# Performance work log

Hardware: AMD Instinct MI355X
Metric: run time of the kernel (lower is better)

## Reference

```python
import jax, jax.numpy as jnp
import numpy as np

NUM_TOPICS = 50
NUM_TIMES = 12
VOCAB1 = 5000
VOCAB2 = 2000
T_HIDDEN = 400
RHO = 300
DELTA = 0.005
BATCH = 32


def setup_inputs() -> dict:
    key = jax.random.key(0)
    ks = jax.random.split(key, 16)
    s = 0.02
    V = VOCAB1 + VOCAB2
    d = {}
    d["bows"] = jax.random.uniform(ks[0], (BATCH, NUM_TIMES, V), jnp.float32)
    d["normalized_bows"] = jax.random.uniform(ks[1], (BATCH, NUM_TIMES, V), jnp.float32)
    d["qmap_w"] = jax.random.normal(ks[2], (T_HIDDEN, V), jnp.float32) * s
    d["qmap_b"] = jnp.zeros((T_HIDDEN,), jnp.float32)
    d["lstm_wih0"] = jax.random.normal(ks[3], (4 * T_HIDDEN, T_HIDDEN), jnp.float32) * s
    d["lstm_whh0"] = jax.random.normal(ks[4], (4 * T_HIDDEN, T_HIDDEN), jnp.float32) * s
    d["lstm_bih0"] = jnp.zeros((4 * T_HIDDEN,), jnp.float32)
    d["lstm_bhh0"] = jnp.zeros((4 * T_HIDDEN,), jnp.float32)
    d["lstm_wih1"] = jax.random.normal(ks[5], (4 * T_HIDDEN, T_HIDDEN), jnp.float32) * s
    d["lstm_whh1"] = jax.random.normal(ks[6], (4 * T_HIDDEN, T_HIDDEN), jnp.float32) * s
    d["lstm_bih1"] = jnp.zeros((4 * T_HIDDEN,), jnp.float32)
    d["lstm_bhh1"] = jnp.zeros((4 * T_HIDDEN,), jnp.float32)
    d["mu_theta_w"] = jax.random.normal(ks[7], (NUM_TOPICS, T_HIDDEN + NUM_TOPICS), jnp.float32) * s
    d["mu_theta_b"] = jnp.zeros((NUM_TOPICS,), jnp.float32)
    d["ls_theta_w"] = jax.random.normal(ks[8], (NUM_TOPICS, T_HIDDEN + NUM_TOPICS), jnp.float32) * s
    d["ls_theta_b"] = jnp.zeros((NUM_TOPICS,), jnp.float32)
    d["mu_q_alpha"] = jax.random.normal(ks[9], (NUM_TOPICS, NUM_TIMES, RHO), jnp.float32)
    d["logsigma_q_alpha"] = jax.random.normal(ks[10], (NUM_TOPICS, NUM_TIMES, RHO), jnp.float32)
    d["rho1_w"] = jax.random.normal(ks[11], (VOCAB1, RHO), jnp.float32) * s
    d["rho1_b"] = jnp.zeros((VOCAB1,), jnp.float32)
    d["rho2_w"] = jax.random.normal(ks[12], (VOCAB2, RHO), jnp.float32) * s
    d["rho2_b"] = jnp.zeros((VOCAB2,), jnp.float32)
    return d


def _kl(qm, qls, pm, pls):
    # 0.5 * sum_last[ (exp(qls) + (qm-pm)^2) / (exp(pls)+1e-6) - 1 + pls - qls ], mean over rest
    t = (jnp.exp(qls) + (qm - pm) ** 2) / (jnp.exp(pls) + 1e-6) - 1.0 + pls - qls
    return (0.5 * jnp.sum(t, axis=-1)).mean()


def _lstm(x, layers):
    # x: [B, T, H]; PyTorch gate order i, f, g, o; eval mode -> no inter-layer dropout
    for wih, whh, bih, bhh in layers:
        B = x.shape[0]
        H = whh.shape[1]

        def step(carry, xt, wih=wih, whh=whh, bih=bih, bhh=bhh):
            h, c = carry
            g = xt @ wih.T + bih + h @ whh.T + bhh
            i, f, gg, o = jnp.split(g, 4, axis=-1)
            c = jax.nn.sigmoid(f) * c + jax.nn.sigmoid(i) * jnp.tanh(gg)
            h = jax.nn.sigmoid(o) * jnp.tanh(c)
            return (h, c), h

        init = (jnp.zeros((B, H), x.dtype), jnp.zeros((B, H), x.dtype))
        _, hs = jax.lax.scan(step, init, jnp.swapaxes(x, 0, 1))  # [T, B, H]
        x = jnp.swapaxes(hs, 0, 1)
    return x


def _likelihood(beta, theta, bows_v, key):
    # beta: [T, K, V], theta: [T, B, K], bows_v: [B, T, V]
    def body(carry, xs):
        t, beta_t, theta_t, bows_t = xs
        # pi[b,v,k] = softmax_k( beta[k,v] * theta[b,k] )
        pi = jax.nn.softmax(theta_t[:, None, :] * beta_t.T[None, :, :], axis=-1)  # [B,V,K]
        g = jax.random.gumbel(jax.random.fold_in(key, t), pi.shape, pi.dtype)
        # F.gumbel_softmax with pi as the "logits", tau=1, hard=True (straight-through)
        y_soft = jax.nn.softmax(pi + g, axis=-1)
        y_hard = jax.nn.one_hot(jnp.argmax(y_soft, axis=-1), pi.shape[-1], dtype=pi.dtype)
        z = y_hard + y_soft - jax.lax.stop_gradient(y_soft)
        kld = (-(z * jnp.log(theta_t)[:, None, :]).sum(-1).mean()
               - (((pi * z).sum(-1) * (jnp.log(pi) * z).sum(-1)).sum(-1)).mean())
        beta_z = beta_t * z.mean(0).T   # [K, V]
        theta_z = theta_t * z.mean(1)   # [B, K]
        ll = (jnp.log(theta_z @ beta_z) * bows_t).sum(1).mean()
        return carry, (kld, ll)

    ts = jnp.arange(beta.shape[0])
    _, (klds, lls) = jax.lax.scan(jax.checkpoint(body), 0,
                                  (ts, beta, theta, jnp.swapaxes(bows_v, 0, 1)))
    return klds.sum(), lls.sum()


def _forward(bows, normalized_bows, qmap_w, qmap_b,
             lstm_wih0, lstm_whh0, lstm_bih0, lstm_bhh0,
             lstm_wih1, lstm_whh1, lstm_bih1, lstm_bhh1,
             mu_theta_w, mu_theta_b, ls_theta_w, ls_theta_b,
             mu_q_alpha, logsigma_q_alpha, rho1_w, rho1_b, rho2_w, rho2_b):
    B = bows.shape[0]
    log_delta = jnp.log(jnp.float32(DELTA))

    # ---- get_theta (eval mode: reparameterize -> mu, dropout off) ----
    inp = normalized_bows @ qmap_w.T + qmap_b                       # [B,T,H]
    out = _lstm(inp, [(lstm_wih0, lstm_whh0, lstm_bih0, lstm_bhh0),
                      (lstm_wih1, lstm_whh1, lstm_bih1, lstm_bhh1)])
    out_t = jnp.swapaxes(out, 0, 1)                                 # [T,B,H]
    inp0 = jnp.concatenate([out_t[0], jnp.zeros((B, NUM_TOPICS), out.dtype)], axis=-1)
    mu0 = inp0 @ mu_theta_w.T + mu_theta_b
    ls0 = inp0 @ ls_theta_w.T + ls_theta_b
    kl0 = _kl(mu0, ls0, jnp.zeros_like(mu0), jnp.zeros_like(ls0))

    def tstep(z_prev, o_t):
        inp_t = jnp.concatenate([o_t, z_prev], axis=-1)
        mu = inp_t @ mu_theta_w.T + mu_theta_b
        ls = inp_t @ ls_theta_w.T + ls_theta_b
        klt = _kl(mu, ls, z_prev, jnp.full_like(mu, log_delta))
        return mu, (mu, klt)

    _, (zs_rest, kls) = jax.lax.scan(tstep, mu0, out_t[1:])
    zs = jnp.concatenate([mu0[None], zs_rest], axis=0)              # [T,B,K]
    kld_theta = kl0 + kls.sum()
    theta = jax.nn.softmax(zs, axis=-1)

    # ---- get_alpha (eval mode: alpha_t = mu_q_alpha[:,t]) -> fully vectorized ----
    q_mu = jnp.swapaxes(mu_q_alpha, 0, 1)                           # [T,K,R]
    q_ls = jnp.swapaxes(logsigma_q_alpha, 0, 1)
    p_mu = jnp.concatenate([jnp.zeros_like(q_mu[:1]), q_mu[:-1]], axis=0)
    p_ls = jnp.concatenate([jnp.zeros_like(q_ls[:1]), jnp.full_like(q_ls[1:], log_delta)], axis=0)
    kl_tk = 0.5 * jnp.sum((jnp.exp(q_ls) + (q_mu - p_mu) ** 2) / (jnp.exp(p_ls) + 1e-6)
                          - 1.0 + p_ls - q_ls, axis=-1)             # [T,K]
    kld_alpha = kl_tk.mean(-1).sum()
    alpha = q_mu

    # ---- get_beta ----
    beta1 = jax.nn.softmax(jnp.einsum('tkr,vr->tkv', alpha, rho1_w) + rho1_b, axis=-1)
    beta2 = jax.nn.softmax(jnp.einsum('tkr,vr->tkv', alpha, rho2_w) + rho2_b, axis=-1)

    # ---- decode ----
    key = jax.random.key(42)
    kld_z1, ll1 = _likelihood(beta1, theta, bows[:, :, :VOCAB1], jax.random.fold_in(key, 1))
    kld_z2, ll2 = _likelihood(beta2, theta, bows[:, :, -VOCAB2:], jax.random.fold_in(key, 2))
    recon_loss = -ll1 - ll2
    return jnp.stack([recon_loss, kld_theta, kld_z1, kld_z2, kld_alpha])


def reference(bows, normalized_bows, qmap_w, qmap_b,
              lstm_wih0, lstm_whh0, lstm_bih0, lstm_bhh0,
              lstm_wih1, lstm_whh1, lstm_bih1, lstm_bhh1,
              mu_theta_w, mu_theta_b, ls_theta_w, ls_theta_b,
              mu_q_alpha, logsigma_q_alpha, rho1_w, rho1_b, rho2_w, rho2_b):
    return _forward(bows, normalized_bows, qmap_w, qmap_b,
                    lstm_wih0, lstm_whh0, lstm_bih0, lstm_bhh0,
                    lstm_wih1, lstm_whh1, lstm_bih1, lstm_bhh1,
                    mu_theta_w, mu_theta_b, ls_theta_w, ls_theta_b,
                    mu_q_alpha, logsigma_q_alpha, rho1_w, rho1_b, rho2_w, rho2_b)
```

## Files before the change

kernel.cpp:

```cpp
#include <hip/hip_runtime.h>

#define LOG_DELTA (-5.2983174f)
#define LOG50     (3.9120230054f)

typedef __attribute__((ext_vector_type(8))) short short8v;
typedef __attribute__((ext_vector_type(4))) float f32x4;

constexpr size_t OFF_C1G1  = 0;
constexpr size_t OFF_C1G2  = 19200;
constexpr size_t OFF_ACCS  = 38400;
constexpr size_t OFF_C0G   = 38416;
constexpr size_t OFF_BETA  = OFF_C0G  + 4200000;
constexpr size_t OFF_ALPHAT= OFF_BETA + 4200000;
constexpr size_t OFF_INP   = OFF_ALPHAT + 180000;
constexpr size_t OFF_X0    = OFF_INP  + 153600;
constexpr size_t OFF_OUT0  = OFF_X0   + 614400;
constexpr size_t OFF_X1    = OFF_OUT0 + 153600;
constexpr size_t OFF_OUT1  = OFF_X1   + 614400;
constexpr size_t OFF_CST   = OFF_OUT1 + 153600;
constexpr size_t OFF_MUH   = OFF_CST  + 12800;
constexpr size_t OFF_THETA = OFF_MUH  + 38400;
constexpr size_t OFF_LTH   = OFF_THETA+ 19200;
constexpr size_t OFF_MUW4  = OFF_LTH  + 19200;
constexpr size_t OFF_LSW4  = OFF_MUW4 + 20000;
constexpr size_t OFF_RS    = OFF_LTH  + 3300;
constexpr size_t OFF_W0T   = OFF_C0G;
constexpr size_t OFF_W1T   = OFF_C0G + 640000;
constexpr size_t OFF_WIH1T = OFF_C0G + 1280000;
constexpr size_t OFF_NBBF  = OFF_C0G + 1920000;
constexpr size_t OFF_R1BF  = OFF_C0G + 3271680;
constexpr size_t OFF_QWBF  = OFF_BETA;
constexpr size_t OFF_W0BF  = OFF_BETA + 1408000;
constexpr size_t OFF_CST1  = OFF_X1;
constexpr size_t OFF_ALBF  = OFF_X1 + 12800;
constexpr size_t OFF_R2BF  = OFF_X1 + 108800;

__device__ __forceinline__ float wsum64(float x){
  #pragma unroll
  for (int o = 32; o; o >>= 1) x += __shfl_down(x, o);
  return x;
}
__device__ __forceinline__ float u01(unsigned int x){
  x ^= x >> 16; x *= 0x7feb352dU;
  x ^= x >> 15; x *= 0x846ca68bU;
  x ^= x >> 16;
  return ((float)x + 0.5f) * (1.0f/4294967296.0f);
}
__device__ __forceinline__ unsigned short f2bf(float x){
  unsigned int u = __float_as_uint(x);
  u += 0x7FFFu + ((u >> 16) & 1u);
  return (unsigned short)(u >> 16);
}
__device__ __forceinline__ ushort4 f4bf(float4 v){
  ushort4 r;
  r.x = f2bf(v.x); r.y = f2bf(v.y); r.z = f2bf(v.z); r.w = f2bf(v.w);
  return r;
}

__global__ void prep_misc(float* __restrict__ ws,
    const float* __restrict__ muW, const float* __restrict__ lsW,
    const float* __restrict__ qmu,
    const float* __restrict__ bi0, const float* __restrict__ bh0,
    const float* __restrict__ bi1, const float* __restrict__ bh1,
    const float* __restrict__ mb,  const float* __restrict__ lb,
    const float* __restrict__ qb,
    const float* __restrict__ whh0, const float* __restrict__ whh1,
    const float* __restrict__ wih1,
    const float* __restrict__ nbows, const float* __restrict__ qmap_w,
    const float* __restrict__ wih0,
    const float* __restrict__ rho1w, const float* __restrict__ rho2w)
{
  float* zbase = ws + OFF_C1G1;
  float* muW4  = ws + OFF_MUW4;
  float* lsW4  = ws + OFF_LSW4;
  unsigned short* albf = (unsigned short*)(ws + OFF_ALBF);
  float* bsum0 = ws + OFF_LTH;
  float* bsum1 = ws + OFF_LTH + 1600;
  float* mlb   = ws + OFF_LTH + 3200;
  float* rs    = ws + OFF_RS;
  unsigned int* inbz = (unsigned int*)(ws + OFF_INP);
  float* inpf  = ws + OFF_ALPHAT;
  float* w0T   = ws + OFF_W0T;
  float* w1T   = ws + OFF_W1T;
  float* wi1T  = ws + OFF_WIH1T;
  unsigned short* nbbf = (unsigned short*)(ws + OFF_NBBF);
  unsigned short* qwbf = (unsigned short*)(ws + OFF_QWBF);
  unsigned short* w0bf = (unsigned short*)(ws + OFF_W0BF);
  unsigned short* r1bf = (unsigned short*)(ws + OFF_R1BF);
  unsigned short* r2bf = (unsigned short*)(ws + OFF_R2BF);
  const float4 z4 = {0.f, 0.f, 0.f, 0.f};

  for (long long un = blockIdx.x*blockDim.x + threadIdx.x; un < 2713337LL;
       un += (long long)gridDim.x*blockDim.x){
    if (un < 9604){
      int j = (int)un * 4;
      if (j + 3 < 38416) *(float4*)&zbase[j] = z4;
      else { for (int q = 0; q < 4 && j+q < 38416; ++q) zbase[j+q] = 0.f; }
    }
    else if (un < 14604){
      int j = (int)(un - 9604) * 4;
      int k = j / 400, c = j % 400;
      const float* s = &muW[k*450 + c];
      float4 v = {s[0], s[1], s[2], s[3]};
      *(float4*)&muW4[j] = v;
    }
    else if (un < 19604){
      int j = (int)(un - 14604) * 4;
      int k = j / 400, c = j % 400;
      const float* s = &lsW[k*450 + c];
      float4 v = {s[0], s[1], s[2], s[3]};
      *(float4*)&lsW4[j] = v;
    }
    else if (un < 67604){
      int j = (int)(un - 19604) * 4;
      int m = j / 320, r = j % 320;
      int t = m / 50, k = m % 50;
      ushort4 o = {0,0,0,0};
      if (r < 300) o = f4bf(*(const float4*)&qmu[((size_t)k*12 + t)*300 + r]);
      *(ushort4*)&albf[j] = o;
    }
    else if (un < 68004){
      int j = (int)(un - 67604) * 4;
      float4 a = *(const float4*)&bi0[j], b = *(const float4*)&bh0[j];
      float4 v = {a.x+b.x, a.y+b.y, a.z+b.z, a.w+b.w};
      *(float4*)&bsum0[j] = v;
    }
    else if (un < 68404){
      int j = (int)(un - 68004) * 4;
      float4 a = *(const float4*)&bi1[j], b = *(const float4*)&bh1[j];
      float4 v = {a.x+b.x, a.y+b.y, a.z+b.z, a.w+b.w};
      *(float4*)&bsum1[j] = v;
    }
    else if (un < 68429){
      int j = (int)(un - 68404) * 4;
      #pragma unroll
      for (int q = 0; q < 4; ++q){
        int jj = j + q;
        mlb[jj] = (jj < 50) ? mb[jj] : lb[jj-50];
      }
    }
    else if (un < 68729){
      int j = (int)(un - 68429) * 4;
      *(float4*)&rs[j] = z4;
    }
    else if (un < 88697){
      int j = (int)(un - 68729) * 4;
      *(uint4*)&inbz[j] = make_uint4(0u,0u,0u,0u);
    }
    else if (un < 568697){
      long long rel = un - 88697;
      int half = (int)(rel / 160000);
      int j = (int)(rel % 160000) * 4;
      int r = j / 1600, c = j % 1600;
      int u = c >> 2;
      const float* src = (half == 0) ? whh0 : (half == 1) ? whh1 : wih1;
      float* dst = (half == 0) ? w0T : (half == 1) ? w1T : wi1T;
      float4 v = { src[((size_t)(0*400 + u))*400 + r],
                   src[((size_t)(1*400 + u))*400 + r],
                   src[((size_t)(2*400 + u))*400 + r],
                   src[((size_t)(3*400 + u))*400 + r] };
      *(float4*)&dst[j] = v;
    }
    else if (un < 1244537){
      int j = (int)(un - 568697) * 4;
      int row = j / 7040, v = j % 7040;
      ushort4 o = {0,0,0,0};
      if (v < 7000) o = f4bf(*(const float4*)&nbows[(size_t)row*7000 + v]);
      *(ushort4*)&nbbf[j] = o;
    }
    else if (un < 1948537){
      int j = (int)(un - 1244537) * 4;
      int row = j / 7040, v = j % 7040;
      ushort4 o = {0,0,0,0};
      if (v < 7000) o = f4bf(*(const float4*)&qmap_w[(size_t)row*7000 + v]);
      *(ushort4*)&qwbf[j] = o;
    }
    else if (un < 2114937){
      int j = (int)(un - 1948537) * 4;
      int row = j / 416, r = j % 416;
      ushort4 o = {0,0,0,0};
      if (r < 400) o = f4bf(*(const float4*)&wih0[(size_t)row*400 + r]);
      *(ushort4*)&w0bf[j] = o;
    }
    else if (un < 2514937){
      int j = (int)(un - 2114937) * 4;
      int row = j / 320, r = j % 320;
      ushort4 o = {0,0,0,0};
      if (r < 300) o = f4bf(*(const float4*)&rho1w[(size_t)row*300 + r]);
      *(ushort4*)&r1bf[j] = o;
    }
    else if (un < 2674937){
      int j = (int)(un - 2514937) * 4;
      int row = j / 320, r = j % 320;
      ushort4 o = {0,0,0,0};
      if (r < 300) o = f4bf(*(const float4*)&rho2w[(size_t)row*300 + r]);
      *(ushort4*)&r2bf[j] = o;
    }
    else {
      int j = (int)(un - 2674937) * 4;
      int c = j % 400;
      *(float4*)&inpf[j] = *(const float4*)&qb[c];
    }
  }
}

__global__ __launch_bounds__(256) void gemm_bf16(
    const unsigned short* __restrict__ A, int lda,
    const unsigned short* __restrict__ B, int ldb,
    float* __restrict__ Cf, unsigned short* __restrict__ Cbf,
    float* __restrict__ Cacc, int ldc,
    int M, int N, int Kp, int kchunk,
    const float* __restrict__ bias, float* __restrict__ rowsum)
{
  __shared__ unsigned short As[64][40];
  __shared__ unsigned short Bs[64][40];
  __shared__ float sexp[64];
  const int tid = threadIdx.x;
  const int m0 = blockIdx.y * 64, n0 = blockIdx.x * 64;
  const int kbeg = blockIdx.z * kchunk;
  const int kend = min(Kp, kbeg + kchunk);
  const int wave = tid >> 6, lane = tid & 63;
  const int wm = (wave >> 1) * 32, wn = (wave & 1) * 32;
  const int ra = tid >> 2, ck = (tid & 3) << 3;
  const int fr = lane & 15, fo = (lane >> 4) << 3;
  if (rowsum && tid < 64) sexp[tid] = 0.f;

  f32x4 acc00 = {0.f,0.f,0.f,0.f}, acc01 = {0.f,0.f,0.f,0.f};
  f32x4 acc10 = {0.f,0.f,0.f,0.f}, acc11 = {0.f,0.f,0.f,0.f};
  int4 pa, pb;
  {
    int rA = m0 + ra, rB = n0 + ra;
    pa = (rA < M) ? *(const int4*)&A[(size_t)rA*lda + kbeg + ck] : make_int4(0,0,0,0);
    pb = (rB < N) ? *(const int4*)&B[(size_t)rB*ldb + kbeg + ck] : make_int4(0,0,0,0);
  }
  for (int k0 = kbeg; k0 < kend; k0 += 32){
    *(int4*)&As[ra][ck] = pa;
    *(int4*)&Bs[ra][ck] = pb;
    __syncthreads();
    if (k0 + 32 < kend){
      int rA = m0 + ra, rB = n0 + ra;
      pa = (rA < M) ? *(const int4*)&A[(size_t)rA*lda + k0 + 32 + ck] : make_int4(0,0,0,0);
      pb = (rB < N) ? *(const int4*)&B[(size_t)rB*ldb + k0 + 32 + ck] : make_int4(0,0,0,0);
    }
    short8v a0 = *(const short8v*)&As[wm      + fr][fo];
    short8v a1 = *(const short8v*)&As[wm + 16 + fr][fo];
    short8v b0 = *(const short8v*)&Bs[wn      + fr][fo];
    short8v b1 = *(const short8v*)&Bs[wn + 16 + fr][fo];
    acc00 = __builtin_amdgcn_mfma_f32_16x16x32_bf16(a0, b0, acc00, 0, 0, 0);
    acc01 = __builtin_amdgcn_mfma_f32_16x16x32_bf16(a0, b1, acc01, 0, 0, 0);
    acc10 = __builtin_amdgcn_mfma_f32_16x16x32_bf16(a1, b0, acc10, 0, 0, 0);
    acc11 = __builtin_amdgcn_mfma_f32_16x16x32_bf16(a1, b1, acc11, 0, 0, 0);
    __syncthreads();
  }
  const int rbase = (lane >> 4) << 2;
  auto epi = [&](f32x4 ac0, f32x4 ac1, int mi){
    #pragma unroll
    for (int reg = 0; reg < 4; ++reg){
      const int lr = wm + mi*16 + rbase + reg;
      const int gr = m0 + lr;
      float ex = 0.f;
      {
        int gc = n0 + wn + fr;
        if (gr < M && gc < N){
          if (Cacc) atomicAdd(&Cacc[(size_t)gr*ldc + gc], ac0[reg]);
          else {
            float val = ac0[reg] + (bias ? bias[gc] : 0.f);
            if (Cbf) Cbf[(size_t)gr*ldc + gc] = f2bf(val);
            else     Cf [(size_t)gr*ldc + gc] = val;
            if (rowsum) ex += __expf(val);
          }
        }
      }
      {
        int gc = n0 + wn + 16 + fr;
        if (gr < M && gc < N){
          if (Cacc) atomicAdd(&Cacc[(size_t)gr*ldc + gc], ac1[reg]);
          else {
            float val = ac1[reg] + (bias ? bias[gc] : 0.f);
            if (Cbf) Cbf[(size_t)gr*ldc + gc] = f2bf(val);
            else     Cf [(size_t)gr*ldc + gc] = val;
            if (rowsum) ex += __expf(val);
          }
        }
      }
      if (rowsum){
        ex += __shfl_xor(ex, 1); ex += __shfl_xor(ex, 2);
        ex += __shfl_xor(ex, 4); ex += __shfl_xor(ex, 8);
        if (fr == 0 && gr < M) atomicAdd(&sexp[lr], ex);
      }
    }
  };
  epi(acc00, acc01, 0);
  epi(acc10, acc11, 1);
  if (rowsum){
    __syncthreads();
    if (tid < 64 && m0 + tid < M) atomicAdd(&rowsum[m0 + tid], sexp[tid]);
  }
}

__global__ void cvt_inp(const float* __restrict__ inpf, unsigned short* __restrict__ inpbf){
  int un = blockIdx.x*blockDim.x + threadIdx.x;
  if (un < 38400){
    int j = un * 4;
    int r = j / 400, c = j % 400;
    ushort4 o = f4bf(*(const float4*)&inpf[j]);
    *(ushort4*)&inpbf[r*416 + c] = o;
  }
}

__device__ __forceinline__ float4 g4(const float* __restrict__ base, int row, int nrows,
                                     int ld, int k, int kend){
  float4 v; v.x = v.y = v.z = v.w = 0.f;
  if (row < nrows){
    const float* q = base + (size_t)row*ld + k;
    if (k + 3 < kend) v = *(const float4*)q;
  }
  return v;
}
__global__ __launch_bounds__(256) void gemm_f32(
    const float* __restrict__ A, int lda,
    const float* __restrict__ B, int ldb,
    float* __restrict__ C, int ldc,
    int M, int N, int K,
    const float* __restrict__ bias)
{
  __shared__ __align__(16) float As[16][68];
  __shared__ __align__(16) float Bs[16][68];
  const int tid = threadIdx.x;
  const int m0 = blockIdx.y * 64, n0 = blockIdx.x * 64;
  const int lm  = tid >> 2;
  const int lkq = (tid & 3) << 2;
  const int ty = tid >> 4, tx = tid & 15;
  float acc[4][4];
  #pragma unroll
  for (int i=0;i<4;++i)
    #pragma unroll
    for (int j=0;j<4;++j) acc[i][j] = 0.f;
  for (int k0 = 0; k0 < K; k0 += 16){
    float4 av = g4(A, m0+lm, M, lda, k0+lkq, K);
    float4 bv = g4(B, n0+lm, N, ldb, k0+lkq, K);
    As[lkq+0][lm]=av.x; As[lkq+1][lm]=av.y; As[lkq+2][lm]=av.z; As[lkq+3][lm]=av.w;
    Bs[lkq+0][lm]=bv.x; Bs[lkq+1][lm]=bv.y; Bs[lkq+2][lm]=bv.z; Bs[lkq+3][lm]=bv.w;
    __syncthreads();
    #pragma unroll
    for (int kk = 0; kk < 16; ++kk){
      const float4 a = *(const float4*)&As[kk][ty<<2];
      const float4 b = *(const float4*)&Bs[kk][tx<<2];
      float ar[4] = {a.x,a.y,a.z,a.w};
      float br[4] = {b.x,b.y,b.z,b.w};
      #pragma unroll
      for (int i=0;i<4;++i)
        #pragma unroll
        for (int j=0;j<4;++j) acc[i][j] = fmaf(ar[i], br[j], acc[i][j]);
    }
    __syncthreads();
  }
  const int om = m0 + (ty<<2), on = n0 + (tx<<2);
  #pragma unroll
  for (int i=0;i<4;++i)
    #pragma unroll
    for (int j=0;j<4;++j)
      if (om+i < M && on+j < N)
        C[(size_t)(om+i)*ldc + (on+j)] = acc[i][j] + (bias ? bias[on+j] : 0.f);
}

__global__ __launch_bounds__(256) void lstm_pipe(
    const float* __restrict__ X0,    const float* __restrict__ w0T,
    const float* __restrict__ wi1T,  const float* __restrict__ w1T,
    const float* __restrict__ bsum1,
    float* __restrict__ hs0, float* __restrict__ hs1,
    float* __restrict__ cst0, float* __restrict__ cst1, int step)
{
  __shared__ __align__(16) float4 hq4[100*32];
  __shared__ __align__(16) float4 red4[4][32][2];
  const int tid = threadIdx.x;
  const int rh = tid >> 6;
  const int b  = (tid & 63) >> 1;
  const int ul = tid & 1;
  const int rq0 = rh * 25;

  if (blockIdx.x < 200){
    const int t = step;
    if (t >= 12) return;
    const int U0 = blockIdx.x * 2;
    const int u = U0 + ul;
    if (t > 0){
      for (int i = tid; i < 3200; i += 256){
        int bb = i & 31, rq = i >> 5;
        hq4[rq*32 + bb] = *(const float4*)&hs0[((size_t)(bb*12 + (t-1)))*400 + rq*4];
      }
      __syncthreads();
      const float* wcol = w0T + (size_t)u*4;
      float4 acc = {0.f,0.f,0.f,0.f};
      #pragma unroll 5
      for (int rq = rq0; rq < rq0 + 25; ++rq){
        float4 h4 = hq4[rq*32 + b];
        float hr[4] = {h4.x, h4.y, h4.z, h4.w};
        #pragma unroll
        for (int dr = 0; dr < 4; ++dr){
          float4 w4 = *(const float4*)&wcol[(size_t)(rq*4 + dr)*1600];
          acc.x = fmaf(hr[dr], w4.x, acc.x);
          acc.y = fmaf(hr[dr], w4.y, acc.y);
          acc.z = fmaf(hr[dr], w4.z, acc.z);
          acc.w = fmaf(hr[dr], w4.w, acc.w);
        }
      }
      red4[rh][b][ul] = acc;
    }
    __syncthreads();
    if (tid < 64){
      const int bb = tid >> 1, uu = U0 + (tid & 1);
      float4 a = {0.f,0.f,0.f,0.f};
      if (t > 0){
        #pragma unroll
        for (int w = 0; w < 4; ++w){
          float4 r = red4[w][bb][tid & 1];
          a.x += r.x; a.y += r.y; a.z += r.z; a.w += r.w;
        }
      }
      const size_t xrow = ((size_t)bb*12 + t)*1600;
      float gi = a.x + X0[xrow          + uu];
      float gf = a.y + X0[xrow +  400   + uu];
      float gg = a.z + X0[xrow +  800   + uu];
      float go = a.w + X0[xrow + 1200   + uu];
      float ii = 1.f/(1.f + expf(-gi));
      float ff = 1.f/(1.f + expf(-gf));
      float tg = tanhf(gg);
      float oo = 1.f/(1.f + expf(-go));
      float c = (t == 0) ? 0.f : cst0[bb*400 + uu];
      c = ff*c + ii*tg;
      cst0[bb*400 + uu] = c;
      hs0[((size_t)bb*12 + t)*400 + uu] = oo * tanhf(c);
    }
  } else {
    const int t = step - 1;
    if (t < 0) return;
    const int U0 = (blockIdx.x - 200) * 2;
    const int u = U0 + ul;
    float4 acc = {0.f,0.f,0.f,0.f};
    for (int i = tid; i < 3200; i += 256){
      int bb = i & 31, rq = i >> 5;
      hq4[rq*32 + bb] = *(const float4*)&hs0[((size_t)(bb*12 + t))*400 + rq*4];
    }
    __syncthreads();
    {
      const float* wcol = wi1T + (size_t)u*4;
      #pragma unroll 5
      for (int rq = rq0; rq < rq0 + 25; ++rq){
        float4 h4 = hq4[rq*32 + b];
        float hr[4] = {h4.x, h4.y, h4.z, h4.w};
        #pragma unroll
        for (int dr = 0; dr < 4; ++dr){
          float4 w4 = *(const float4*)&wcol[(size_t)(rq*4 + dr)*1600];
          acc.x = fmaf(hr[dr], w4.x, acc.x);
          acc.y = fmaf(hr[dr], w4.y, acc.y);
          acc.z = fmaf(hr[dr], w4.z, acc.z);
          acc.w = fmaf(hr[dr], w4.w, acc.w);
        }
      }
    }
    __syncthreads();
    if (t > 0){
      for (int i = tid; i < 3200; i += 256){
        int bb = i & 31, rq = i >> 5;
        hq4[rq*32 + bb] = *(const float4*)&hs1[((size_t)(bb*12 + (t-1)))*400 + rq*4];
      }
    }
    __syncthreads();
    if (t > 0){
      const float* wcol = w1T + (size_t)u*4;
      #pragma unroll 5
      for (int rq = rq0; rq < rq0 + 25; ++rq){
        float4 h4 = hq4[rq*32 + b];
        float hr[4] = {h4.x, h4.y, h4.z, h4.w};
        #pragma unroll
        for (int dr = 0; dr < 4; ++dr){
          float4 w4 = *(const float4*)&wcol[(size_t)(rq*4 + dr)*1600];
          acc.x = fmaf(hr[dr], w4.x, acc.x);
          acc.y = fmaf(hr[dr], w4.y, acc.y);
          acc.z = fmaf(hr[dr], w4.z, acc.z);
          acc.w = fmaf(hr[dr], w4.w, acc.w);
        }
      }
    }
    red4[rh][b][ul] = acc;
    __syncthreads();
    if (tid < 64){
      const int bb = tid >> 1, uu = U0 + (tid & 1);
      float4 a = {0.f,0.f,0.f,0.f};
      #pragma unroll
      for (int w = 0; w < 4; ++w){
        float4 r = red4[w][bb][tid & 1];
        a.x += r.x; a.y += r.y; a.z += r.z; a.w += r.w;
      }
      float gi = a.x + bsum1[        uu];
      float gf = a.y + bsum1[ 400 + uu];
      float gg = a.z + bsum1[ 800 + uu];
      float go = a.w + bsum1[1200 + uu];
      float ii = 1.f/(1.f + expf(-gi));
      float ff = 1.f/(1.f + expf(-gf));
      float tg = tanhf(gg);
      float oo = 1.f/(1.f + expf(-go));
      float c = (t == 0) ? 0.f : cst1[bb*400 + uu];
      c = ff*c + ii*tg;
      cst1[bb*400 + uu] = c;
      hs1[((size_t)bb*12 + t)*400 + uu] = oo * tanhf(c);
    }
  }
}

__global__ __launch_bounds__(512) void theta_par(
    const float* __restrict__ muH2,
    const float* __restrict__ muW, const float* __restrict__ lsW,
    float* __restrict__ theta, float* __restrict__ accs)
{
  __shared__ float zsall[12][8][50];
  __shared__ float wm[50][51], wl[50][51];
  __shared__ float ktot;
  const int tid = threadIdx.x;
  const int b0 = blockIdx.x * 8;
  for (int i = tid; i < 2500; i += 512){
    int k = i / 50, j = i % 50;
    wm[k][j] = muW[k*450 + 400 + j];
    wl[k][j] = lsW[k*450 + 400 + j];
  }
  if (tid == 0) ktot = 0.f;
  __syncthreads();
  const float dd = expf(LOG_DELTA) + 1e-6f;
  for (int t = 0; t < 12; ++t){
    float kpart = 0.f;
    if (tid < 400){
      int bl = tid / 50, k = tid % 50, b = b0 + bl;
      float m = muH2[((size_t)b*12 + t)*100 + k];
      float l = muH2[((size_t)b*12 + t)*100 + 50 + k];
      float zp = 0.f;
      if (t > 0){
        zp = zsall[t-1][bl][k];
        float sm = 0.f, sl = 0.f;
        #pragma unroll 5
        for (int j = 0; j < 50; ++j){
          float z = zsall[t-1][bl][j];
          sm = fmaf(z, wm[k][j], sm);
          sl = fmaf(z, wl[k][j], sl);
        }
        m += sm; l += sl;
      }
      zsall[t][bl][k] = m;
      float denom = (t > 0) ? dd : (1.f + 1e-6f);
      float pls = (t > 0) ? LOG_DELTA : 0.f;
      float d = m - zp;
      kpart += (expf(l) + d*d)/denom - 1.f + pls - l;
    }
    kpart = wsum64(kpart);
    if ((tid & 63) == 0) atomicAdd(&ktot, 0.5f * kpart / 32.f);
    __syncthreads();
  }
  for (int rr = tid; rr < 96; rr += 512){
    int t = rr >> 3, bl = rr & 7, b = b0 + bl;
    float m = -3.0e38f;
    for (int k = 0; k < 50; ++k) m = fmaxf(m, zsall[t][bl][k]);
    float S = 0.f;
    for (int k = 0; k < 50; ++k) S += expf(zsall[t][bl][k] - m);
    float inv = 1.f/S;
    for (int k = 0; k < 50; ++k)
      theta[((size_t)t*32 + b)*50 + k] = expf(zsall[t][bl][k] - m) * inv;
  }
  if (tid == 0) atomicAdd(&accs[6], ktot);
}

__global__ void kld_alpha_k(const float* __restrict__ qmu, const float* __restrict__ qls,
                            float* __restrict__ accs){
  const int t = blockIdx.x / 50, k = blockIdx.x % 50;
  const size_t base  = ((size_t)k*12 + t)*300;
  const size_t pbase = ((size_t)k*12 + (t-1))*300;
  const float dd  = (t > 0) ? (expf(LOG_DELTA) + 1e-6f) : (1.f + 1e-6f);
  const float pls = (t > 0) ? LOG_DELTA : 0.f;
  float s = 0.f;
  for (int r = threadIdx.x; r < 300; r += 64){
    float qm = qmu[base + r], ql = qls[base + r];
    float pm = (t > 0) ? qmu[pbase + r] : 0.f;
    float d = qm - pm;
    s += (expf(ql) + d*d)/dd - 1.f + pls - ql;
  }
  s = wsum64(s);
  if (threadIdx.x == 0) atomicAdd(&accs[7], 0.5f * s / 50.f);
}

__global__ __launch_bounds__(256) void pass1(
    const float* __restrict__ blog, const float* __restrict__ rs,
    const float* __restrict__ theta,
    float* __restrict__ bzg,
    float* __restrict__ c1g1, float* __restrict__ c1g2,
    float* __restrict__ accs)
{
  const int t = blockIdx.y;
  const int v0 = blockIdx.x * 64;
  __shared__ float th[32][50];
  __shared__ float be[50][64];
  __shared__ float c0s[64][50];
  __shared__ unsigned int c1p[2][32][25];
  __shared__ float rlog[2][50];
  __shared__ float kred[4];
  const int tid = threadIdx.x;

  if (tid < 100){
    int p = tid / 50, k = tid % 50;
    rlog[p][k] = __logf(rs[p*600 + t*50 + k]);
  }
  float lg[13];
  #pragma unroll
  for (int j = 0; j < 13; ++j){
    int i = tid + j*256;
    lg[j] = -40.f;
    if (i < 3200){
      int k = i >> 6, vl = i & 63, v = v0 + vl;
      if (v < 7000) lg[j] = blog[((size_t)t*50 + k)*7000 + v];
    }
  }
  #pragma unroll
  for (int j = 0; j < 7; ++j){
    int i = tid + j*256;
    if (i < 1600) th[i/50][i%50] = theta[(size_t)t*1600 + i];
  }
  #pragma unroll
  for (int j = 0; j < 13; ++j){
    int i = tid + j*256;
    if (i < 3200) ((float*)c0s)[i] = 0.f;
  }
  #pragma unroll
  for (int j = 0; j < 7; ++j){
    int i = tid + j*256;
    if (i < 1600) ((unsigned int*)c1p)[i] = 0u;
  }
  if (tid < 4) kred[tid] = 0.f;
  __syncthreads();
  #pragma unroll
  for (int j = 0; j < 13; ++j){
    int i = tid + j*256;
    if (i < 3200){
      int k = i >> 6, vl = i & 63, v = v0 + vl;
      int p = (v >= 5000);
      be[k][vl] = __expf(lg[j] - rlog[p][k]);
    }
  }
  __syncthreads();

  const int b = tid >> 3, sub = tid & 7;

  float sx[8], mx[8];
  #pragma unroll
  for (int i = 0; i < 8; ++i){ sx[i] = 0.f; mx[i] = 0.f; }
  for (int k = 0; k < 50; ++k){
    float tk = th[b][k];
    #pragma unroll
    for (int i = 0; i < 8; ++i){
      float x = tk * be[k][sub + 8*i];
      sx[i] += x;
      mx[i] = fmaxf(mx[i], x);
    }
  }
  float inv[8], lS1[8], bnd[8];
  #pragma unroll
  for (int i = 0; i < 8; ++i){
    inv[i] = 1.f / (50.f + sx[i]);
    lS1[i] = LOG50 + sx[i] * 0.02f;
    bnd[i] = (1.f + mx[i]) * inv[i];
  }

  int ks[8]; float xs[8];
  unsigned fmask = 0;
  const int vbase = (t*32 + b)*7000 + v0 + sub;
  #pragma unroll
  for (int i = 0; i < 8; ++i){
    ks[i] = 0; xs[i] = 0.f;
    if (v0 + sub + 8*i >= 7000) fmask |= 1u << i;
  }
  int round = 0;
  while (true){
    const unsigned roff = (unsigned)round * 0x9E3779B9u;
    #pragma unroll
    for (int i = 0; i < 8; ++i){
      if (!((fmask >> i) & 1u)){
        const unsigned bse = (unsigned)(vbase + 8*i) * 2u;
        float u1 = u01(bse + roff);
        float u2 = u01(bse + 1u + roff);
        int kp = min((int)(u1 * 50.f), 49);
        float x  = th[b][kp] * be[kp][sub + 8*i];
        float pi = (1.f + x) * inv[i];
        float y  = pi - bnd[i];
        float ap = 1.f + y + 0.5f*y*y;
        if (u2 <= ap || round >= 7){
          ks[i] = kp; xs[i] = x; fmask |= 1u << i;
        }
      }
    }
    ++round;
    if (__all(fmask == 255u)) break;
  }

  float kA1 = 0.f, kB1 = 0.f, kA2 = 0.f, kB2 = 0.f;
  #pragma unroll
  for (int i = 0; i < 8; ++i){
    const int vl = sub + 8*i, v = v0 + vl;
    if (v < 7000){
      float pis  = (1.f + xs[i]) * inv[i];
      float lpis = xs[i] - lS1[i];
      float lt   = __logf(th[b][ks[i]]);
      if (v >= 5000){ kA2 += lt; kB2 += pis*lpis; }
      else          { kA1 += lt; kB1 += pis*lpis; }
      atomicAdd(&c0s[vl][ks[i]], 1.f);
      atomicAdd(&c1p[(v >= 5000) ? 1 : 0][b][ks[i] >> 1],
                (ks[i] & 1) ? 65536u : 1u);
    }
  }
  kA1 = wsum64(kA1); kB1 = wsum64(kB1); kA2 = wsum64(kA2); kB2 = wsum64(kB2);
  if ((tid & 63) == 0){
    atomicAdd(&kred[0], kA1); atomicAdd(&kred[1], kB1);
    atomicAdd(&kred[2], kA2); atomicAdd(&kred[3], kB2);
  }
  __syncthreads();
  #pragma unroll
  for (int j = 0; j < 13; ++j){
    int i = tid + j*256;
    if (i < 3200){
      int k = i >> 6, vl = i & 63, v = v0 + vl;
      if (v < 7000)
        bzg[(size_t)t*350000 + (size_t)k*7000 + v] = be[k][vl] * c0s[vl][k] * (1.f/32.f);
    }
  }
  for (int i = tid; i < 1600; i += 256){
    int b2 = i / 50, k2 = i % 50;
    unsigned w1 = c1p[0][b2][k2 >> 1];
    unsigned w2 = c1p[1][b2][k2 >> 1];
    unsigned cnt1 = (k2 & 1) ? (w1 >> 16) : (w1 & 0xFFFFu);
    unsigned cnt2 = (k2 & 1) ? (w2 >> 16) : (w2 & 0xFFFFu);
    if (cnt1) atomicAdd(&c1g1[(size_t)t*1600 + i], (float)cnt1);
    if (cnt2) atomicAdd(&c1g2[(size_t)t*1600 + i], (float)cnt2);
  }
  if (tid < 4) atomicAdd(&accs[tid], kred[tid]);
}

__global__ __launch_bounds__(256) void pass2(
    const float* __restrict__ bzg, const float* __restrict__ theta,
    const float* __restrict__ c1g1, const float* __restrict__ c1g2,
    const float* __restrict__ bows, float* __restrict__ accs)
{
  const int t = blockIdx.y, v0 = blockIdx.x * 64;
  __shared__ float tz[2][32][50];
  __shared__ float bzs[50][64];
  __shared__ float sr[2];
  const int tid = threadIdx.x;
  if (tid < 2) sr[tid] = 0.f;
  for (int i = tid; i < 1600; i += 256){
    int b = i / 50, k = i % 50;
    float th_ = theta[(size_t)t*1600 + i];
    tz[0][b][k] = th_ * c1g1[(size_t)t*1600 + i] * (1.f/5000.f);
    tz[1][b][k] = th_ * c1g2[(size_t)t*1600 + i] * (1.f/2000.f);
  }
  for (int i = tid; i < 3200; i += 256){
    int k = i >> 6, vl = i & 63, v = v0 + vl;
    bzs[k][vl] = (v < 7000) ? bzg[(size_t)t*350000 + (size_t)k*7000 + v] : 0.f;
  }
  __syncthreads();

  const int b = tid >> 3, sub = tid & 7;
  int part[8];
  #pragma unroll
  for (int i = 0; i < 8; ++i) part[i] = (v0 + sub + 8*i >= 5000);
  float dot[8];
  #pragma unroll
  for (int i = 0; i < 8; ++i) dot[i] = 0.f;
  for (int k = 0; k < 50; ++k){
    float t0 = tz[0][b][k], t1 = tz[1][b][k];
    #pragma unroll
    for (int i = 0; i < 8; ++i)
      dot[i] = fmaf(part[i] ? t1 : t0, bzs[k][sub + 8*i], dot[i]);
  }
  float s1 = 0.f, s2 = 0.f;
  #pragma unroll
  for (int i = 0; i < 8; ++i){
    const int v = v0 + sub + 8*i;
    if (v < 7000){
      const float w = bows[((size_t)b*12 + t)*7000 + v];
      const float l = __logf(dot[i]) * w;
      if (part[i]) s2 += l; else s1 += l;
    }
  }
  s1 = wsum64(s1); s2 = wsum64(s2);
  if ((tid & 63) == 0){ atomicAdd(&sr[0], s1); atomicAdd(&sr[1], s2); }
  __syncthreads();
  if (tid < 2) atomicAdd(&accs[4 + tid], sr[tid]);
}

__global__ void finalize_k(const float* __restrict__ accs, float* __restrict__ out){
  if (threadIdx.x == 0 && blockIdx.x == 0){
    out[0] = -(accs[4] + accs[5]) * (1.f/32.f);
    out[1] = accs[6];
    out[2] = -accs[0]/(32.f*5000.f) - accs[1]/32.f;
    out[3] = -accs[2]/(32.f*2000.f) - accs[3]/32.f;
    out[4] = accs[7];
  }
}

extern "C" void kernel_launch(void* const* d_in, const int* in_sizes, int n_in,
                              void* d_out, int out_size, void* d_ws, size_t ws_size,
                              hipStream_t stream)
{
  const float* bows   = (const float*)d_in[0];
  const float* nbows  = (const float*)d_in[1];
  const float* qmap_w = (const float*)d_in[2];
  const float* qmap_b = (const float*)d_in[3];
  const float* wih0   = (const float*)d_in[4];
  const float* whh0   = (const float*)d_in[5];
  const float* bih0   = (const float*)d_in[6];
  const float* bhh0   = (const float*)d_in[7];
  const float* wih1   = (const float*)d_in[8];
  const float* whh1   = (const float*)d_in[9];
  const float* bih1   = (const float*)d_in[10];
  const float* bhh1   = (const float*)d_in[11];
  const float* muW    = (const float*)d_in[12];
  const float* muB    = (const float*)d_in[13];
  const float* lsW    = (const float*)d_in[14];
  const float* lsB    = (const float*)d_in[15];
  const float* qmu    = (const float*)d_in[16];
  const float* qlsa   = (const float*)d_in[17];
  const float* rho1w  = (const float*)d_in[18];
  const float* rho1b  = (const float*)d_in[19];
  const float* rho2w  = (const float*)d_in[20];
  const float* rho2b  = (const float*)d_in[21];

  float* ws  = (float*)d_ws;
  float* out = (float*)d_out;

  float* c1g1  = ws + OFF_C1G1;
  float* c1g2  = ws + OFF_C1G2;
  float* accs  = ws + OFF_ACCS;
  float* bzg   = ws + OFF_C0G;
  float* beta  = ws + OFF_BETA;
  float* inpf  = ws + OFF_ALPHAT;
  float* X0    = ws + OFF_X0;
  float* hs0   = ws + OFF_OUT0;
  float* hs1   = ws + OFF_OUT1;
  float* cst0  = ws + OFF_CST;
  float* cst1  = ws + OFF_CST1;
  float* muH2  = ws + OFF_MUH;
  float* theta = ws + OFF_THETA;
  float* muW4  = ws + OFF_MUW4;
  float* bsum0 = ws + OFF_LTH;
  float* bsum1 = ws + OFF_LTH + 1600;
  float* mlb   = ws + OFF_LTH + 3200;
  float* rs    = ws + OFF_RS;
  unsigned short* nbbf  = (unsigned short*)(ws + OFF_NBBF);
  unsigned short* qwbf  = (unsigned short*)(ws + OFF_QWBF);
  unsigned short* inpbf = (unsigned short*)(ws + OFF_INP);
  unsigned short* w0bf  = (unsigned short*)(ws + OFF_W0BF);
  unsigned short* albf  = (unsigned short*)(ws + OFF_ALBF);
  unsigned short* r1bf  = (unsigned short*)(ws + OFF_R1BF);
  unsigned short* r2bf  = (unsigned short*)(ws + OFF_R2BF);
  float* w0T  = ws + OFF_W0T;
  float* w1T  = ws + OFF_W1T;
  float* wi1T = ws + OFF_WIH1T;

  prep_misc<<<2048, 256, 0, stream>>>(ws, muW, lsW, qmu, bih0, bhh0, bih1, bhh1,
                                      muB, lsB, qmap_b, whh0, whh1, wih1,
                                      nbows, qmap_w, wih0, rho1w, rho2w);
  kld_alpha_k<<<600, 64, 0, stream>>>(qmu, qlsa, accs);

  gemm_bf16<<<dim3(7,6,10), 256, 0, stream>>>(nbbf, 7040, qwbf, 7040,
                                              nullptr, nullptr, inpf, 400,
                                              384, 400, 7040, 704, nullptr, nullptr);
  cvt_inp<<<150, 256, 0, stream>>>(inpf, inpbf);

  gemm_bf16<<<dim3(25,6,1), 256, 0, stream>>>(inpbf, 416, w0bf, 416,
                                              X0, nullptr, nullptr, 1600,
                                              384, 1600, 416, 416, bsum0, nullptr);
  for (int i = 0; i < 13; ++i)
    lstm_pipe<<<400, 256, 0, stream>>>(X0, w0T, wi1T, w1T, bsum1,
                                       hs0, hs1, cst0, cst1, i);

  gemm_f32<<<dim3(2,6), 256, 0, stream>>>(hs1, 400, muW4, 400, muH2, 100,
                                          384, 100, 400, mlb);
  theta_par<<<4, 512, 0, stream>>>(muH2, muW, lsW, theta, accs);

  gemm_bf16<<<dim3(79,10,1), 256, 0, stream>>>(albf, 320, r1bf, 320,
                                               beta, nullptr, nullptr, 7000,
                                               600, 5000, 320, 320, rho1b, rs);
  gemm_bf16<<<dim3(32,10,1), 256, 0, stream>>>(albf, 320, r2bf, 320,
                                               beta + 5000, nullptr, nullptr, 7000,
                                               600, 2000, 320, 320, rho2b, rs + 600);

  pass1<<<dim3(110,12), 256, 0, stream>>>(beta, rs, theta, bzg, c1g1, c1g2, accs);
  pass2<<<dim3(110,12), 256, 0, stream>>>(bzg, theta, c1g1, c1g2, bows, accs);

  finalize_k<<<1, 64, 0, stream>>>(accs, out);
}
```

Before: 442.5 us.

## Remap pass1/pass2 columns to contiguous float4 reads, pack counts, widen theta_par grid

theta_par now runs one 64-thread block per batch row across 32 blocks instead of 4 blocks of 512 threads, which spreads the serial 12-step recurrence over more CUs and drops the shared-memory atomic. In pass1 and pass2 each thread now owns 8 contiguous vocab columns instead of a stride-8 set, so the shared-memory beta rows and the bows row can be read with float4 loads. Pass1 also packs its per-column topic counts into 8-bit fields of unsigned ints, shrinking shared memory and its zeroing. The column remap changes which RNG indices each element uses within a block, and the 8-bit counters assume at most 255 hits per column.

```diff
diff --git a/kernel.cpp b/kernel.cpp
--- a/kernel.cpp
+++ b/kernel.cpp
@@ -509,63 +509,62 @@
   }
 }
 
-__global__ __launch_bounds__(512) void theta_par(
+__global__ __launch_bounds__(64) void theta_par(
     const float* __restrict__ muH2,
     const float* __restrict__ muW, const float* __restrict__ lsW,
     float* __restrict__ theta, float* __restrict__ accs)
 {
-  __shared__ float zsall[12][8][50];
   __shared__ float wm[50][51], wl[50][51];
-  __shared__ float ktot;
+  __shared__ float zs[12][50];
   const int tid = threadIdx.x;
-  const int b0 = blockIdx.x * 8;
-  for (int i = tid; i < 2500; i += 512){
+  const int b = blockIdx.x;
+  for (int i = tid; i < 2500; i += 64){
     int k = i / 50, j = i % 50;
     wm[k][j] = muW[k*450 + 400 + j];
     wl[k][j] = lsW[k*450 + 400 + j];
   }
-  if (tid == 0) ktot = 0.f;
   __syncthreads();
   const float dd = expf(LOG_DELTA) + 1e-6f;
+  float kacc = 0.f;
   for (int t = 0; t < 12; ++t){
     float kpart = 0.f;
-    if (tid < 400){
-      int bl = tid / 50, k = tid % 50, b = b0 + bl;
+    if (tid < 50){
+      int k = tid;
       float m = muH2[((size_t)b*12 + t)*100 + k];
       float l = muH2[((size_t)b*12 + t)*100 + 50 + k];
       float zp = 0.f;
       if (t > 0){
-        zp = zsall[t-1][bl][k];
+        zp = zs[t-1][k];
         float sm = 0.f, sl = 0.f;
         #pragma unroll 5
         for (int j = 0; j < 50; ++j){
-          float z = zsall[t-1][bl][j];
+          float z = zs[t-1][j];
           sm = fmaf(z, wm[k][j], sm);
           sl = fmaf(z, wl[k][j], sl);
         }
         m += sm; l += sl;
       }
-      zsall[t][bl][k] = m;
+      zs[t][k] = m;
       float denom = (t > 0) ? dd : (1.f + 1e-6f);
       float pls = (t > 0) ? LOG_DELTA : 0.f;
       float d = m - zp;
-      kpart += (expf(l) + d*d)/denom - 1.f + pls - l;
+      kpart = (expf(l) + d*d)/denom - 1.f + pls - l;
     }
     kpart = wsum64(kpart);
-    if ((tid & 63) == 0) atomicAdd(&ktot, 0.5f * kpart / 32.f);
-    __syncthreads();
-  }
-  for (int rr = tid; rr < 96; rr += 512){
-    int t = rr >> 3, bl = rr & 7, b = b0 + bl;
+    if (tid == 0) kacc += 0.5f * kpart / 32.f;
+    __syncthreads();
+  }
+  if (tid < 12){
+    int t = tid;
     float m = -3.0e38f;
-    for (int k = 0; k < 50; ++k) m = fmaxf(m, zsall[t][bl][k]);
+    for (int k = 0; k < 50; ++k) m = fmaxf(m, zs[t][k]);
     float S = 0.f;
-    for (int k = 0; k < 50; ++k) S += expf(zsall[t][bl][k] - m);
+    for (int k = 0; k < 50; ++k) S += expf(zs[t][k] - m);
     float inv = 1.f/S;
     for (int k = 0; k < 50; ++k)
-      theta[((size_t)t*32 + b)*50 + k] = expf(zsall[t][bl][k] - m) * inv;
-  }
-  if (tid == 0) atomicAdd(&accs[6], ktot);
+      theta[((size_t)t*32 + b)*50 + k] = expf(zs[t][k] - m) * inv;
+  }
+  if (tid == 0) atomicAdd(&accs[6], kacc);
 }
 
 __global__ void kld_alpha_k(const float* __restrict__ qmu, const float* __restrict__ qls,
@@ -596,8 +595,8 @@
   const int t = blockIdx.y;
   const int v0 = blockIdx.x * 64;
   __shared__ float th[32][50];
-  __shared__ float be[50][64];
-  __shared__ float c0s[64][50];
+  __shared__ __align__(16) float be[50][64];
+  __shared__ unsigned int c0p[64][13];
   __shared__ unsigned int c1p[2][32][25];
   __shared__ float rlog[2][50];
   __shared__ float kred[4];
@@ -622,11 +621,7 @@
     int i = tid + j*256;
     if (i < 1600) th[i/50][i%50] = theta[(size_t)t*1600 + i];
   }
-  #pragma unroll
-  for (int j = 0; j < 13; ++j){
-    int i = tid + j*256;
-    if (i < 3200) ((float*)c0s)[i] = 0.f;
-  }
+  for (int i = tid; i < 832; i += 256) ((unsigned int*)c0p)[i] = 0u;
   #pragma unroll
   for (int j = 0; j < 7; ++j){
     int i = tid + j*256;
@@ -646,15 +641,19 @@
   __syncthreads();
 
   const int b = tid >> 3, sub = tid & 7;
+  const int vb = sub << 3;
 
   float sx[8], mx[8];
   #pragma unroll
   for (int i = 0; i < 8; ++i){ sx[i] = 0.f; mx[i] = 0.f; }
   for (int k = 0; k < 50; ++k){
     float tk = th[b][k];
+    float4 q0 = *(const float4*)&be[k][vb];
+    float4 q1 = *(const float4*)&be[k][vb + 4];
+    float bv[8] = {q0.x,q0.y,q0.z,q0.w,q1.x,q1.y,q1.z,q1.w};
     #pragma unroll
     for (int i = 0; i < 8; ++i){
-      float x = tk * be[k][sub + 8*i];
+      float x = tk * bv[i];
       sx[i] += x;
       mx[i] = fmaxf(mx[i], x);
     }
@@ -669,11 +668,11 @@
 
   int ks[8]; float xs[8];
   unsigned fmask = 0;
-  const int vbase = (t*32 + b)*7000 + v0 + sub;
+  const int vbase = (t*32 + b)*7000 + v0 + vb;
   #pragma unroll
   for (int i = 0; i < 8; ++i){
     ks[i] = 0; xs[i] = 0.f;
-    if (v0 + sub + 8*i >= 7000) fmask |= 1u << i;
+    if (v0 + vb + i >= 7000) fmask |= 1u << i;
   }
   int round = 0;
   while (true){
@@ -681,11 +680,11 @@
     #pragma unroll
     for (int i = 0; i < 8; ++i){
       if (!((fmask >> i) & 1u)){
-        const unsigned bse = (unsigned)(vbase + 8*i) * 2u;
+        const unsigned bse = (unsigned)(vbase + i) * 2u;
         float u1 = u01(bse + roff);
         float u2 = u01(bse + 1u + roff);
         int kp = min((int)(u1 * 50.f), 49);
-        float x  = th[b][kp] * be[kp][sub + 8*i];
+        float x  = th[b][kp] * be[kp][vb + i];
         float pi = (1.f + x) * inv[i];
         float y  = pi - bnd[i];
         float ap = 1.f + y + 0.5f*y*y;
@@ -701,14 +700,14 @@
   float kA1 = 0.f, kB1 = 0.f, kA2 = 0.f, kB2 = 0.f;
   #pragma unroll
   for (int i = 0; i < 8; ++i){
-    const int vl = sub + 8*i, v = v0 + vl;
+    const int vl = vb + i, v = v0 + vl;
     if (v < 7000){
       float pis  = (1.f + xs[i]) * inv[i];
       float lpis = xs[i] - lS1[i];
       float lt   = __logf(th[b][ks[i]]);
       if (v >= 5000){ kA2 += lt; kB2 += pis*lpis; }
       else          { kA1 += lt; kB1 += pis*lpis; }
-      atomicAdd(&c0s[vl][ks[i]], 1.f);
+      atomicAdd(&c0p[vl][ks[i] >> 2], 1u << (8*(ks[i] & 3)));
       atomicAdd(&c1p[(v >= 5000) ? 1 : 0][b][ks[i] >> 1],
                 (ks[i] & 1) ? 65536u : 1u);
     }
@@ -724,8 +723,10 @@
     int i = tid + j*256;
     if (i < 3200){
       int k = i >> 6, vl = i & 63, v = v0 + vl;
-      if (v < 7000)
-        bzg[(size_t)t*350000 + (size_t)k*7000 + v] = be[k][vl] * c0s[vl][k] * (1.f/32.f);
+      if (v < 7000){
+        float cnt = (float)((c0p[vl][k >> 2] >> (8*(k & 3))) & 0xFFu);
+        bzg[(size_t)t*350000 + (size_t)k*7000 + v] = be[k][vl] * cnt * (1.f/32.f);
+      }
     }
   }
   for (int i = tid; i < 1600; i += 256){
@@ -747,7 +748,7 @@
 {
   const int t = blockIdx.y, v0 = blockIdx.x * 64;
   __shared__ float tz[2][32][50];
-  __shared__ float bzs[50][64];
+  __shared__ __align__(16) float bzs[50][64];
   __shared__ float sr[2];
   const int tid = threadIdx.x;
   if (tid < 2) sr[tid] = 0.f;
@@ -764,25 +765,40 @@
   __syncthreads();
 
   const int b = tid >> 3, sub = tid & 7;
+  const int vb = sub << 3;
   int part[8];
   #pragma unroll
-  for (int i = 0; i < 8; ++i) part[i] = (v0 + sub + 8*i >= 5000);
+  for (int i = 0; i < 8; ++i) part[i] = (v0 + vb + i >= 5000);
   float dot[8];
   #pragma unroll
   for (int i = 0; i < 8; ++i) dot[i] = 0.f;
   for (int k = 0; k < 50; ++k){
     float t0 = tz[0][b][k], t1 = tz[1][b][k];
+    float4 q0 = *(const float4*)&bzs[k][vb];
+    float4 q1 = *(const float4*)&bzs[k][vb + 4];
+    float bv[8] = {q0.x,q0.y,q0.z,q0.w,q1.x,q1.y,q1.z,q1.w};
     #pragma unroll
     for (int i = 0; i < 8; ++i)
-      dot[i] = fmaf(part[i] ? t1 : t0, bzs[k][sub + 8*i], dot[i]);
+      dot[i] = fmaf(part[i] ? t1 : t0, bv[i], dot[i]);
+  }
+  float w8[8];
+  const size_t brow = ((size_t)b*12 + t)*7000;
+  if (v0 + vb + 7 < 7000){
+    float4 wa = *(const float4*)&bows[brow + v0 + vb];
+    float4 wb = *(const float4*)&bows[brow + v0 + vb + 4];
+    w8[0]=wa.x; w8[1]=wa.y; w8[2]=wa.z; w8[3]=wa.w;
+    w8[4]=wb.x; w8[5]=wb.y; w8[6]=wb.z; w8[7]=wb.w;
+  } else {
+    #pragma unroll
+    for (int i = 0; i < 8; ++i)
+      w8[i] = (v0 + vb + i < 7000) ? bows[brow + v0 + vb + i] : 0.f;
   }
   float s1 = 0.f, s2 = 0.f;
   #pragma unroll
   for (int i = 0; i < 8; ++i){
-    const int v = v0 + sub + 8*i;
+    const int v = v0 + vb + i;
     if (v < 7000){
-      const float w = bows[((size_t)b*12 + t)*7000 + v];
-      const float l = __logf(dot[i]) * w;
+      const float l = __logf(dot[i]) * w8[i];
       if (part[i]) s2 += l; else s1 += l;
     }
   }
@@ -880,7 +896,7 @@
 
   gemm_f32<<<dim3(2,6), 256, 0, stream>>>(hs1, 400, muW4, 400, muH2, 100,
                                           384, 100, 400, mlb);
-  theta_par<<<4, 512, 0, stream>>>(muH2, muW, lsW, theta, accs);
+  theta_par<<<32, 64, 0, stream>>>(muH2, muW, lsW, theta, accs);
 
   gemm_bf16<<<dim3(79,10,1), 256, 0, stream>>>(albf, 320, r1bf, 320,
                                                beta, nullptr, nullptr, 7000,
```

Measured after the change: 433.7 us. -2.0%, faster.
